# Kernel optimization log

Hardware: AMD Instinct MI355X
Metric: run time of the kernel (lower is better)

The kernel has to match this reference:

```python
import jax, jax.numpy as jnp
import numpy as np

N_NODES = 50000
N_RELS = 100000
N_TRIPLES = 100000
D = 512          # node_dim == rel_dim
H = 768          # hidden_dim
NUM_LAYERS = 3
B = 16           # number of images (segments)
EPS = 1e-5


def setup_inputs() -> dict:
    key = jax.random.key(0)
    ks = jax.random.split(key, 12)
    node_feats = jax.random.normal(ks[0], (N_NODES, D), dtype=jnp.float32)
    rel_feats = jax.random.normal(ks[1], (N_RELS, D), dtype=jnp.float32)
    subj = jax.random.randint(ks[2], (N_TRIPLES,), 0, N_NODES)
    rel = jax.random.randint(ks[3], (N_TRIPLES,), 0, N_RELS)
    obj = jax.random.randint(ks[4], (N_TRIPLES,), 0, N_NODES)
    triples = jnp.stack([subj, rel, obj], axis=1).astype(jnp.int64)
    obj_to_img = jnp.sort(jax.random.randint(ks[5], (N_NODES,), 0, B))
    obj_to_img = obj_to_img.at[-1].set(B - 1)  # pin batch_size = B (torch uses max+1)
    obj_to_img = obj_to_img.astype(jnp.int64)
    s = 0.02
    params = dict(
        node_in_w=jax.random.normal(ks[6], (H, D), dtype=jnp.float32) * s,
        node_in_b=jnp.zeros((H,), dtype=jnp.float32),
        rel_in_w=jax.random.normal(ks[7], (H, D), dtype=jnp.float32) * s,
        rel_in_b=jnp.zeros((H,), dtype=jnp.float32),
        proj_w=jax.random.normal(ks[8], (NUM_LAYERS, H, 2 * H), dtype=jnp.float32) * s,
        proj_b=jnp.zeros((NUM_LAYERS, H), dtype=jnp.float32),
        ln_node_g=jnp.ones((H,), dtype=jnp.float32),
        ln_node_b=jnp.zeros((H,), dtype=jnp.float32),
        ln_rel_g=jnp.ones((H,), dtype=jnp.float32),
        ln_rel_b=jnp.zeros((H,), dtype=jnp.float32),
    )
    return dict(node_feats=node_feats, rel_feats=rel_feats, triples=triples,
                obj_to_img=obj_to_img, **params)


def _layer_norm(x, g, b):
    mu = jnp.mean(x, axis=-1, keepdims=True)
    var = jnp.var(x, axis=-1, keepdims=True)
    return (x - mu) * jax.lax.rsqrt(var + EPS) * g + b


def reference(node_feats, rel_feats, triples, obj_to_img,
              node_in_w, node_in_b, rel_in_w, rel_in_b,
              proj_w, proj_b, ln_node_g, ln_node_b, ln_rel_g, ln_rel_b):
    subj_idx, rel_idx, obj_idx = triples[:, 0], triples[:, 1], triples[:, 2]

    node_states = node_feats @ node_in_w.T + node_in_b          # (N_nodes, H)
    rel_states = rel_feats @ rel_in_w.T + rel_in_b               # (N_rels, H)

    for l in range(NUM_LAYERS):
        rel_g = rel_states[rel_idx]                              # (T, H)
        msg_s2o = node_states[subj_idx] + rel_g                  # subject -> object
        msg_o2s = node_states[obj_idx] + rel_g                   # object -> subject
        agg = (jax.ops.segment_sum(msg_s2o, obj_idx, num_segments=N_NODES)
               + jax.ops.segment_sum(msg_o2s, subj_idx, num_segments=N_NODES))
        h = jnp.concatenate([node_states, agg], axis=-1)         # (N_nodes, 2H)
        h = h @ proj_w[l].T + proj_b[l]
        h = jax.nn.silu(h)
        node_states = node_states + h                            # residual (dropout=0)

    node_states = _layer_norm(node_states, ln_node_g, ln_node_b)
    rel_states = _layer_norm(rel_states, ln_rel_g, ln_rel_b)

    sums = jax.ops.segment_sum(node_states, obj_to_img, num_segments=B)
    counts = jax.ops.segment_sum(jnp.ones((N_NODES,), node_states.dtype),
                                 obj_to_img, num_segments=B)
    global_states = sums / jnp.clip(counts, 1.0)[:, None]        # (B, H)
    return node_states, global_states
```

## Files before the change

### kernel.cpp

```cpp
#include <hip/hip_runtime.h>
#include <hip/hip_bf16.h>
#include <math.h>

#define N_NODES   50000
#define N_RELS    100000
#define N_TRIPLES 100000
#define D_IN      512
#define H_DIM     768
#define NUM_LAYERS 3
#define B_IMG     16
#define MP        50176

typedef __attribute__((ext_vector_type(8))) short short8;
typedef __attribute__((ext_vector_type(4))) float f32x4;

typedef const __attribute__((address_space(1))) unsigned int glb_u32;
typedef __attribute__((address_space(3))) unsigned int lds_u32;

__device__ inline short f2bf16s(float f){
  union { __hip_bfloat16 h; unsigned short u; } cv;
  cv.h = __float2bfloat16(f);
  return (short)cv.u;
}
__device__ inline float bf2f(unsigned short u){
  union { unsigned u; float f; } c; c.u = ((unsigned)u)<<16; return c.f;
}
__device__ inline uint2 pack4bf(float4 v){
  uint2 r;
  r.x = ((unsigned)(unsigned short)f2bf16s(v.x)) | (((unsigned)(unsigned short)f2bf16s(v.y))<<16);
  r.y = ((unsigned)(unsigned short)f2bf16s(v.z)) | (((unsigned)(unsigned short)f2bf16s(v.w))<<16);
  return r;
}
__device__ inline float4 unpack4bf(uint2 p){
  float4 v;
  v.x = bf2f((unsigned short)(p.x & 0xffff)); v.y = bf2f((unsigned short)(p.x >> 16));
  v.z = bf2f((unsigned short)(p.y & 0xffff)); v.w = bf2f((unsigned short)(p.y >> 16));
  return v;
}

__global__ void detect_idx64_kernel(const unsigned* __restrict__ tr, int* __restrict__ flag){
  if (threadIdx.x == 0 && blockIdx.x == 0){
    unsigned o = 0;
    for (int k = 0; k < 256; k++) o |= tr[2*k + 1];
    flag[0] = (o == 0) ? 1 : 0;
  }
}

__device__ inline void load_triple(const void* tp, int t, int is64, int& s, int& r, int& o){
  if (is64){
    const long long* p = (const long long*)tp;
    s = (int)p[3*t]; r = (int)p[3*t+1]; o = (int)p[3*t+2];
  } else {
    const int* p = (const int*)tp;
    s = p[3*t]; r = p[3*t+1]; o = p[3*t+2];
  }
  s = (s < 0) ? 0 : (s >= N_NODES ? N_NODES-1 : s);
  o = (o < 0) ? 0 : (o >= N_NODES ? N_NODES-1 : o);
  r = (r < 0) ? 0 : (r >= N_RELS  ? N_RELS-1  : r);
}

__device__ inline int idx_at(const void* p, int i, int is64){
  return is64 ? (int)((const long long*)p)[i] : ((const int*)p)[i];
}

__global__ __launch_bounds__(256)
void hist_kernel(const void* __restrict__ tr, const int* __restrict__ flag,
                 int* __restrict__ deg){
  int t = blockIdx.x*256 + threadIdx.x;
  if (t >= N_TRIPLES) return;
  int s, r, o;
  load_triple(tr, t, flag[0], s, r, o);
  atomicAdd(&deg[o], 1);
  atomicAdd(&deg[s], 1);
}

__global__ __launch_bounds__(1024)
void scan_kernel(const int* __restrict__ deg, int* __restrict__ offs,
                 int* __restrict__ cursor, float* __restrict__ cnt){
  __shared__ int partial[1024];
  int tid = threadIdx.x;
  const int per = (N_NODES + 1023)/1024;
  int start = tid*per, end = start+per; if (end > N_NODES) end = N_NODES;
  if (start > N_NODES) start = N_NODES;
  int s = 0;
  for (int i=start; i<end; i++) s += deg[i];
  partial[tid] = s;
  __syncthreads();
  for (int off=1; off<1024; off<<=1){
    int v = (tid >= off) ? partial[tid-off] : 0;
    __syncthreads();
    partial[tid] += v;
    __syncthreads();
  }
  int run = (tid > 0) ? partial[tid-1] : 0;
  for (int i=start; i<end; i++){
    offs[i] = run; cursor[i] = run; cnt[i] = (float)deg[i];
    run += deg[i];
  }
  if (tid == 1023) offs[N_NODES] = run;
}

__global__ __launch_bounds__(256)
void fill_kernel(const void* __restrict__ tr, const int* __restrict__ flag,
                 int* __restrict__ cursor, int* __restrict__ col_node,
                 int* __restrict__ col_rel){
  int t = blockIdx.x*256 + threadIdx.x;
  if (t >= N_TRIPLES) return;
  int s, r, o;
  load_triple(tr, t, flag[0], s, r, o);
  int p1 = atomicAdd(&cursor[o], 1); col_node[p1] = s; col_rel[p1] = r;
  int p2 = atomicAdd(&cursor[s], 1); col_node[p2] = o; col_rel[p2] = r;
}

__global__ __launch_bounds__(256)
void gather_rel_kernel(const int* __restrict__ offs, const int* __restrict__ col_rel,
                       const float* __restrict__ relf, unsigned short* __restrict__ rfa_bf){
  int v = blockIdx.x*4 + (threadIdx.x >> 6);
  int lane = threadIdx.x & 63;
  float4 a0 = {0,0,0,0}, a1 = {0,0,0,0};
  int lo = offs[v], hi = offs[v+1];
  for (int e=lo; e<hi; e++){
    int r = col_rel[e];
    const float* rp = relf + (size_t)r*D_IN + lane*4;
    float4 x0 = *(const float4*)rp;
    float4 x1 = *(const float4*)(rp + 256);
    a0.x+=x0.x; a0.y+=x0.y; a0.z+=x0.z; a0.w+=x0.w;
    a1.x+=x1.x; a1.y+=x1.y; a1.z+=x1.z; a1.w+=x1.w;
  }
  uint2* out = (uint2*)(rfa_bf + (size_t)v*D_IN);
  out[lane]    = pack4bf(a0);
  out[lane+64] = pack4bf(a1);
}

__global__ __launch_bounds__(256)
void gather_node_bf_kernel(const int* __restrict__ offs, const int* __restrict__ col_node,
                           const unsigned short* __restrict__ seed_bf,
                           const unsigned short* __restrict__ node_bf,
                           unsigned short* __restrict__ agg_bf){
  int v = blockIdx.x*4 + (threadIdx.x >> 6);
  int lane = threadIdx.x & 63;
  const uint2* sp = (const uint2*)(seed_bf + (size_t)v*H_DIM);
  float4 a0 = unpack4bf(sp[lane]);
  float4 a1 = unpack4bf(sp[lane+64]);
  float4 a2 = unpack4bf(sp[lane+128]);
  int lo = offs[v], hi = offs[v+1];
  for (int e=lo; e<hi; e++){
    int u = col_node[e];
    const uint2* np = (const uint2*)(node_bf + (size_t)u*H_DIM);
    float4 x0 = unpack4bf(np[lane]);
    float4 x1 = unpack4bf(np[lane+64]);
    float4 x2 = unpack4bf(np[lane+128]);
    a0.x+=x0.x; a0.y+=x0.y; a0.z+=x0.z; a0.w+=x0.w;
    a1.x+=x1.x; a1.y+=x1.y; a1.z+=x1.z; a1.w+=x1.w;
    a2.x+=x2.x; a2.y+=x2.y; a2.z+=x2.z; a2.w+=x2.w;
  }
  uint2* out = (uint2*)(agg_bf + (size_t)v*H_DIM);
  out[lane]     = pack4bf(a0);
  out[lane+64]  = pack4bf(a1);
  out[lane+128] = pack4bf(a2);
}

__global__ __launch_bounds__(256)
void gather_node_kernel(const int* __restrict__ offs, const int* __restrict__ col_node,
                        const unsigned short* __restrict__ seed_bf,
                        const float* __restrict__ node,
                        unsigned short* __restrict__ agg_bf){
  int v = blockIdx.x*4 + (threadIdx.x >> 6);
  int lane = threadIdx.x & 63;
  const uint2* sp = (const uint2*)(seed_bf + (size_t)v*H_DIM);
  float4 a0 = unpack4bf(sp[lane]);
  float4 a1 = unpack4bf(sp[lane+64]);
  float4 a2 = unpack4bf(sp[lane+128]);
  int lo = offs[v], hi = offs[v+1];
  for (int e=lo; e<hi; e++){
    int u = col_node[e];
    const float* np = node + (size_t)u*H_DIM + lane*4;
    float4 x0 = *(const float4*)np;
    float4 x1 = *(const float4*)(np + 256);
    float4 x2 = *(const float4*)(np + 512);
    a0.x+=x0.x; a0.y+=x0.y; a0.z+=x0.z; a0.w+=x0.w;
    a1.x+=x1.x; a1.y+=x1.y; a1.z+=x1.z; a1.w+=x1.w;
    a2.x+=x2.x; a2.y+=x2.y; a2.z+=x2.z; a2.w+=x2.w;
  }
  uint2* out = (uint2*)(agg_bf + (size_t)v*H_DIM);
  out[lane]     = pack4bf(a0);
  out[lane+64]  = pack4bf(a1);
  out[lane+128] = pack4bf(a2);
}

__device__ inline short8 load_cvt8(const float* __restrict__ p, bool valid){
  short8 r;
  if (valid){
    float4 v0 = *(const float4*)(p);
    float4 v1 = *(const float4*)(p+4);
    r[0]=f2bf16s(v0.x); r[1]=f2bf16s(v0.y); r[2]=f2bf16s(v0.z); r[3]=f2bf16s(v0.w);
    r[4]=f2bf16s(v1.x); r[5]=f2bf16s(v1.y); r[6]=f2bf16s(v1.z); r[7]=f2bf16s(v1.w);
  } else {
    r = (short8)0;
  }
  return r;
}

template<int MODE>
__global__ __launch_bounds__(512)
void gemm_lds(const unsigned short* __restrict__ A1,
              const unsigned short* __restrict__ A2,
              const unsigned short* __restrict__ W,
              const float* __restrict__ bias,
              const float* __restrict__ rowscale,
              float* __restrict__ Cf,
              unsigned short* __restrict__ Cbf,
              int M, int K1, int K2)
{
  __shared__ unsigned short As[256*64];
  __shared__ unsigned short Bs[128*64];
  const int lane = threadIdx.x & 63;
  const int wv   = threadIdx.x >> 6;
  const int llo  = lane & 15, lhi = lane >> 4;
  const int wm   = (wv>>1)*64;
  const int wn   = (wv&1)*64;

  const int nwg  = gridDim.x;
  const int q8   = nwg >> 3, r8 = nwg & 7;
  const int xcd  = blockIdx.x & 7, base = blockIdx.x >> 3;
  const int virt = (xcd < r8 ? xcd*(q8+1) : r8*(q8+1) + (xcd-r8)*q8) + base;
  const int bm   = (virt / 6) * 256;
  const int bn   = (virt % 6) * 128;
  const int KW   = K1 + K2;

  const int srow = lane >> 3;
  const int scol = ((lane & 7) ^ srow) * 8;

  f32x4 acc[4][4];
  #pragma unroll
  for (int i=0;i<4;i++)
    #pragma unroll
    for (int j=0;j<4;j++) acc[i][j] = (f32x4)(0.0f);

  const unsigned short* Wb = W + (size_t)bn*KW;

  for (int k0=0; k0<KW; k0+=64){
    const unsigned short* Asrc; int ak0, astr;
    if (k0 < K1){ Asrc = A1 + (size_t)bm*K1; ak0 = k0;      astr = K1; }
    else        { Asrc = A2 + (size_t)bm*K2; ak0 = k0 - K1; astr = K2; }
    #pragma unroll
    for (int p=0;p<4;p++){
      int c = wv*4 + p;
      int row = c*8 + srow;
      __builtin_amdgcn_global_load_lds(
        (glb_u32*)(Asrc + (size_t)row*astr + ak0 + scol),
        (lds_u32*)(As + c*512), 16, 0, 0);
    }
    #pragma unroll
    for (int p=0;p<2;p++){
      int c = wv*2 + p;
      int row = c*8 + srow;
      __builtin_amdgcn_global_load_lds(
        (glb_u32*)(Wb + (size_t)row*KW + k0 + scol),
        (lds_u32*)(Bs + c*512), 16, 0, 0);
    }
    __syncthreads();
    #pragma unroll
    for (int kk=0; kk<64; kk+=32){
      short8 a[4], b[4];
      #pragma unroll
      for (int i=0;i<4;i++){
        int rowA = wm + i*16 + llo;
        int rowB = wn + i*16 + llo;
        int c16  = lhi + (kk>>3);
        a[i] = *(const short8*)(As + rowA*64 + ((c16 ^ (rowA&7))*8));
        b[i] = *(const short8*)(Bs + rowB*64 + ((c16 ^ (rowB&7))*8));
      }
      #pragma unroll
      for (int i=0;i<4;i++)
        #pragma unroll
        for (int j=0;j<4;j++)
          acc[i][j] = __builtin_amdgcn_mfma_f32_16x16x32_bf16(a[i], b[j], acc[i][j], 0,0,0);
    }
    __syncthreads();
  }

  #pragma unroll
  for (int j=0;j<4;j++){
    int col = bn + wn + j*16 + llo;
    float bv = bias ? bias[col] : 0.0f;
    #pragma unroll
    for (int i=0;i<4;i++){
      #pragma unroll
      for (int r=0;r<4;r++){
        int row = bm + wm + i*16 + lhi*4 + r;
        if (row < M){
          size_t idx = (size_t)row*H_DIM + col;
          float v = acc[i][j][r];
          if (MODE==0){
            v += bv;
            Cf[idx] = v;
            Cbf[idx] = (unsigned short)f2bf16s(v);
          } else if (MODE==2){
            v += rowscale[row]*bv;
            Cbf[idx] = (unsigned short)f2bf16s(v);
          } else {
            v += bv;
            float s = v / (1.0f + __expf(-v));
            float nv = Cf[idx] + s;
            Cf[idx] = nv;
            Cbf[idx] = (unsigned short)f2bf16s(nv);
          }
        }
      }
    }
  }
}

template<int MODE, int ABF>
__global__ __launch_bounds__(256)
void gemm_in(const float* __restrict__ Xf, const unsigned short* __restrict__ Xbf,
             const unsigned short* __restrict__ W,
             const float* __restrict__ bias, const float* __restrict__ rowscale,
             float* __restrict__ Cf, unsigned short* __restrict__ Cbf,
             int M, int Ka)
{
  const int lane = threadIdx.x & 63;
  const int wv   = threadIdx.x >> 6;
  const int llo  = lane & 15, lhi = lane >> 4;
  const int bm   = blockIdx.x*128 + (wv>>1)*64;
  const int bn   = blockIdx.y*128 + (wv&1)*64;

  f32x4 acc[4][4];
  #pragma unroll
  for (int i=0;i<4;i++)
    #pragma unroll
    for (int j=0;j<4;j++) acc[i][j] = (f32x4)(0.0f);

  for (int k0=0;k0<Ka;k0+=32){
    short8 a[4], b[4];
    #pragma unroll
    for (int i=0;i<4;i++){
      int row = bm + i*16 + llo;
      if (ABF) a[i] = (row < M) ? *(const short8*)(Xbf + (size_t)row*Ka + k0 + lhi*8) : (short8)0;
      else     a[i] = load_cvt8(Xf + (size_t)row*Ka + k0 + lhi*8, row < M);
      b[i] = *(const short8*)(W + (size_t)(bn + i*16 + llo)*Ka + k0 + lhi*8);
    }
    #pragma unroll
    for (int i=0;i<4;i++)
      #pragma unroll
      for (int j=0;j<4;j++)
        acc[i][j] = __builtin_amdgcn_mfma_f32_16x16x32_bf16(a[i], b[j], acc[i][j], 0,0,0);
  }

  #pragma unroll
  for (int j=0;j<4;j++){
    int col = bn + j*16 + llo;
    float bv = bias ? bias[col] : 0.0f;
    #pragma unroll
    for (int i=0;i<4;i++){
      #pragma unroll
      for (int r=0;r<4;r++){
        int row = bm + i*16 + lhi*4 + r;
        if (row < M){
          size_t idx = (size_t)row*H_DIM + col;
          float v = acc[i][j][r];
          if (MODE==2){
            v += rowscale[row]*bv;
            Cbf[idx] = (unsigned short)f2bf16s(v);
          } else {
            Cf[idx] = v + bv;
          }
        }
      }
    }
  }
}

__global__ __launch_bounds__(512)
void gemm_layer(float* __restrict__ node,
                const unsigned short* __restrict__ agg_bf,
                const unsigned short* __restrict__ W,
                const float* __restrict__ bias,
                int M)
{
  const int lane = threadIdx.x & 63;
  const int wv   = threadIdx.x >> 6;
  const int llo  = lane & 15, lhi = lane >> 4;
  const int bm   = blockIdx.x*64;
  const int bn   = wv*96;

  f32x4 acc[4][6];
  #pragma unroll
  for (int i=0;i<4;i++)
    #pragma unroll
    for (int j=0;j<6;j++) acc[i][j] = (f32x4)(0.0f);

  for (int k0=0;k0<H_DIM;k0+=32){
    short8 a[4], b[6];
    #pragma unroll
    for (int i=0;i<4;i++){
      int row = bm + i*16 + llo;
      a[i] = load_cvt8(node + (size_t)row*H_DIM + k0 + lhi*8, row < M);
    }
    #pragma unroll
    for (int j=0;j<6;j++)
      b[j] = *(const short8*)(W + (size_t)(bn + j*16 + llo)*(2*H_DIM) + k0 + lhi*8);
    #pragma unroll
    for (int i=0;i<4;i++)
      #pragma unroll
      for (int j=0;j<6;j++)
        acc[i][j] = __builtin_amdgcn_mfma_f32_16x16x32_bf16(a[i], b[j], acc[i][j], 0,0,0);
  }
  for (int k0=0;k0<H_DIM;k0+=32){
    short8 a[4], b[6];
    #pragma unroll
    for (int i=0;i<4;i++){
      int row = bm + i*16 + llo;
      a[i] = (row < M) ? *(const short8*)(agg_bf + (size_t)row*H_DIM + k0 + lhi*8) : (short8)0;
    }
    #pragma unroll
    for (int j=0;j<6;j++)
      b[j] = *(const short8*)(W + (size_t)(bn + j*16 + llo)*(2*H_DIM) + H_DIM + k0 + lhi*8);
    #pragma unroll
    for (int i=0;i<4;i++)
      #pragma unroll
      for (int j=0;j<6;j++)
        acc[i][j] = __builtin_amdgcn_mfma_f32_16x16x32_bf16(a[i], b[j], acc[i][j], 0,0,0);
  }

  __syncthreads();

  #pragma unroll
  for (int j=0;j<6;j++){
    int col = bn + j*16 + llo;
    float bv = bias[col];
    #pragma unroll
    for (int i=0;i<4;i++){
      #pragma unroll
      for (int r=0;r<4;r++){
        int row = bm + i*16 + lhi*4 + r;
        if (row < M){
          size_t idx = (size_t)row*H_DIM + col;
          float v = acc[i][j][r] + bv;
          float s = v / (1.0f + __expf(-v));
          node[idx] += s;
        }
      }
    }
  }
}

__global__ __launch_bounds__(256)
void cast_bf16_kernel(const float* __restrict__ src, unsigned short* __restrict__ dst,
                      long n){
  long i = ((long)blockIdx.x*blockDim.x + threadIdx.x)*8;
  long stride = (long)gridDim.x*blockDim.x*8;
  for (; i < n; i += stride){
    float4 v0 = *(const float4*)(src+i);
    float4 v1 = *(const float4*)(src+i+4);
    short8 o;
    o[0]=f2bf16s(v0.x); o[1]=f2bf16s(v0.y); o[2]=f2bf16s(v0.z); o[3]=f2bf16s(v0.w);
    o[4]=f2bf16s(v1.x); o[5]=f2bf16s(v1.y); o[6]=f2bf16s(v1.z); o[7]=f2bf16s(v1.w);
    *(short8*)(dst+i) = o;
  }
}

__global__ __launch_bounds__(256)
void ln_kernel(const float* __restrict__ x, const float* __restrict__ g,
               const float* __restrict__ b, float* __restrict__ out){
  int row = blockIdx.x;
  int t = threadIdx.x;
  const float* xr = x + (size_t)row*H_DIM;
  float v0 = xr[t], v1 = xr[t+256], v2 = xr[t+512];
  float s  = v0+v1+v2;
  float ss = v0*v0+v1*v1+v2*v2;
  for (int off=32; off>0; off>>=1){
    s  += __shfl_down(s,  off);
    ss += __shfl_down(ss, off);
  }
  __shared__ float rs_[4], rss_[4];
  __shared__ float mu_s, rstd_s;
  int lane = t & 63, wv = t >> 6;
  if (lane==0){ rs_[wv]=s; rss_[wv]=ss; }
  __syncthreads();
  if (t==0){
    float S  = rs_[0]+rs_[1]+rs_[2]+rs_[3];
    float SS = rss_[0]+rss_[1]+rss_[2]+rss_[3];
    float mu = S * (1.0f/768.0f);
    float var = SS * (1.0f/768.0f) - mu*mu;
    mu_s = mu; rstd_s = rsqrtf(var + 1e-5f);
  }
  __syncthreads();
  float mu = mu_s, rstd = rstd_s;
  float* orow = out + (size_t)row*H_DIM;
  orow[t]     = (v0-mu)*rstd*g[t]     + b[t];
  orow[t+256] = (v1-mu)*rstd*g[t+256] + b[t+256];
  orow[t+512] = (v2-mu)*rstd*g[t+512] + b[t+512];
}

__global__ __launch_bounds__(256)
void pool1_kernel(const float* __restrict__ ln, const void* __restrict__ o2i,
                  const int* __restrict__ flag, float* __restrict__ acc){
  const int ROWS = 125;
  int is64 = flag[0];
  int r0 = blockIdx.x*ROWS;
  int t = threadIdx.x;
  float a0=0.f, a1=0.f, a2=0.f;
  int cur = idx_at(o2i, r0, is64);
  cur = (cur < 0) ? 0 : (cur >= B_IMG ? B_IMG-1 : cur);
  for (int r=r0; r<r0+ROWS; r++){
    int img = idx_at(o2i, r, is64);
    img = (img < 0) ? 0 : (img >= B_IMG ? B_IMG-1 : img);
    if (img != cur){
      atomicAdd(&acc[cur*H_DIM + t],       a0);
      atomicAdd(&acc[cur*H_DIM + t + 256], a1);
      atomicAdd(&acc[cur*H_DIM + t + 512], a2);
      a0 = a1 = a2 = 0.f;
      cur = img;
    }
    const float* xr = ln + (size_t)r*H_DIM;
    a0 += xr[t]; a1 += xr[t+256]; a2 += xr[t+512];
  }
  atomicAdd(&acc[cur*H_DIM + t],       a0);
  atomicAdd(&acc[cur*H_DIM + t + 256], a1);
  atomicAdd(&acc[cur*H_DIM + t + 512], a2);
}

__device__ inline int lbound_idx(const void* a, int n, int v, int is64){
  int lo=0, hi=n;
  while (lo<hi){ int m=(lo+hi)>>1; if (idx_at(a,m,is64) < v) lo=m+1; else hi=m; }
  return lo;
}

__global__ __launch_bounds__(256)
void pool2_kernel(const float* __restrict__ acc, const void* __restrict__ o2i,
                  const int* __restrict__ flag, float* __restrict__ gout){
  int is64 = flag[0];
  int img = blockIdx.x;
  int t = threadIdx.x;
  int lo = lbound_idx(o2i, N_NODES, img,   is64);
  int hi = lbound_idx(o2i, N_NODES, img+1, is64);
  float c = (float)(hi-lo);
  if (c < 1.0f) c = 1.0f;
  float inv = 1.0f / c;
  gout[(size_t)img*H_DIM + t]       = acc[img*H_DIM + t]       * inv;
  gout[(size_t)img*H_DIM + t + 256] = acc[img*H_DIM + t + 256] * inv;
  gout[(size_t)img*H_DIM + t + 512] = acc[img*H_DIM + t + 512] * inv;
}

extern "C" void kernel_launch(void* const* d_in, const int* in_sizes, int n_in,
                              void* d_out, int out_size, void* d_ws, size_t ws_size,
                              hipStream_t stream){
  const float* node_feats = (const float*)d_in[0];
  const float* rel_feats  = (const float*)d_in[1];
  const void*  triples    = d_in[2];
  const void*  o2i        = d_in[3];
  const float* node_in_w  = (const float*)d_in[4];
  const float* node_in_b  = (const float*)d_in[5];
  const float* rel_in_w   = (const float*)d_in[6];
  const float* rel_in_b   = (const float*)d_in[7];
  const float* proj_w     = (const float*)d_in[8];
  const float* proj_b     = (const float*)d_in[9];
  const float* ln_g       = (const float*)d_in[10];
  const float* ln_b       = (const float*)d_in[11];

  float* out_nodes  = (float*)d_out;
  float* out_global = (float*)d_out + (size_t)N_NODES*H_DIM;

  const int  tri_blocks = (N_TRIPLES + 255)/256;
  const int  gat_blocks = N_NODES/4;

  size_t off = 0;
  auto alloc = [&](size_t bytes)->void*{
    void* r = (char*)d_ws + off; off += (bytes + 255) & ~(size_t)255; return r;
  };
  unsigned short* w_node     = (unsigned short*)alloc((size_t)H_DIM*D_IN*2);
  unsigned short* w_rel      = (unsigned short*)alloc((size_t)H_DIM*D_IN*2);
  unsigned short* w_proj     = (unsigned short*)alloc((size_t)NUM_LAYERS*H_DIM*2*H_DIM*2);
  unsigned short* rel_agg_bf = (unsigned short*)alloc((size_t)MP*H_DIM*2);
  unsigned short* shr_bf     = (unsigned short*)alloc((size_t)MP*D_IN*2);
  unsigned short* node_bf0   = (unsigned short*)alloc((size_t)MP*H_DIM*2);
  unsigned short* node_bf1   = (unsigned short*)alloc((size_t)MP*H_DIM*2);
  unsigned short* agg_bf     = (unsigned short*)alloc((size_t)MP*H_DIM*2);
  float*          cnt        = (float*)alloc((size_t)N_NODES*4);
  int*            deg        = (int*)alloc((size_t)N_NODES*4);
  int*            offs       = (int*)alloc((size_t)(N_NODES+1)*4);
  int*            cursor     = (int*)alloc((size_t)N_NODES*4);
  int*            col_node   = (int*)alloc((size_t)2*N_TRIPLES*4);
  int*            col_rel    = (int*)alloc((size_t)2*N_TRIPLES*4);
  int*            flag       = (int*)alloc(256);
  float*          pool_acc   = (float*)alloc((size_t)B_IMG*H_DIM*4);
  size_t need_full = off;

  detect_idx64_kernel<<<1,64,0,stream>>>((const unsigned*)triples, flag);
  hipMemsetAsync(deg, 0, (size_t)N_NODES*4, stream);
  hist_kernel<<<tri_blocks,256,0,stream>>>(triples, flag, deg);
  scan_kernel<<<1,1024,0,stream>>>(deg, offs, cursor, cnt);
  fill_kernel<<<tri_blocks,256,0,stream>>>(triples, flag, cursor, col_node, col_rel);
  cast_bf16_kernel<<<512,256,0,stream>>>(node_in_w, w_node, (long)H_DIM*D_IN);
  cast_bf16_kernel<<<512,256,0,stream>>>(rel_in_w,  w_rel,  (long)H_DIM*D_IN);
  cast_bf16_kernel<<<2048,256,0,stream>>>(proj_w, w_proj, (long)NUM_LAYERS*H_DIM*2*H_DIM);

  if (ws_size >= need_full){
    const int gg = (MP/256) * (H_DIM/128);

    cast_bf16_kernel<<<2048,256,0,stream>>>(node_feats, shr_bf, (long)N_NODES*D_IN);
    gemm_lds<0><<<gg,512,0,stream>>>(shr_bf, nullptr, w_node, node_in_b, nullptr,
                                     out_nodes, node_bf0, N_NODES, D_IN, 0);

    gather_rel_kernel<<<gat_blocks,256,0,stream>>>(offs, col_rel, rel_feats, shr_bf);
    gemm_lds<2><<<gg,512,0,stream>>>(shr_bf, nullptr, w_rel, rel_in_b, cnt,
                                     nullptr, rel_agg_bf, N_NODES, D_IN, 0);

    unsigned short* cur = node_bf0;
    unsigned short* nxt = node_bf1;
    for (int l=0; l<NUM_LAYERS; ++l){
      gather_node_bf_kernel<<<gat_blocks,256,0,stream>>>(offs, col_node, rel_agg_bf,
                                                         cur, agg_bf);
      gemm_lds<1><<<gg,512,0,stream>>>(cur, agg_bf,
                                       w_proj + (size_t)l*H_DIM*2*H_DIM,
                                       proj_b + (size_t)l*H_DIM, nullptr,
                                       out_nodes, nxt, N_NODES, H_DIM, H_DIM);
      unsigned short* t = cur; cur = nxt; nxt = t;
    }
  } else {
    size_t off2 = 0;
    auto alloc2 = [&](size_t bytes)->void*{
      void* r = (char*)d_ws + off2; off2 += (bytes + 255) & ~(size_t)255; return r;
    };
    unsigned short* w_node2  = (unsigned short*)alloc2((size_t)H_DIM*D_IN*2);
    unsigned short* w_rel2   = (unsigned short*)alloc2((size_t)H_DIM*D_IN*2);
    unsigned short* w_proj2  = (unsigned short*)alloc2((size_t)NUM_LAYERS*H_DIM*2*H_DIM*2);
    unsigned short* relagg2  = (unsigned short*)alloc2((size_t)N_NODES*H_DIM*2);
    unsigned short* rfa2     = (unsigned short*)alloc2((size_t)N_NODES*D_IN*2);
    unsigned short* agg2     = (unsigned short*)alloc2((size_t)N_NODES*H_DIM*2);
    float* cnt2   = (float*)alloc2((size_t)N_NODES*4);
    int*   deg2   = (int*)alloc2((size_t)N_NODES*4);
    int*   offs2  = (int*)alloc2((size_t)(N_NODES+1)*4);
    int*   cur2   = (int*)alloc2((size_t)N_NODES*4);
    int*   coln2  = (int*)alloc2((size_t)2*N_TRIPLES*4);
    int*   colr2  = (int*)alloc2((size_t)2*N_TRIPLES*4);
    int*   flag2  = (int*)alloc2(256);
    float* pacc2  = (float*)alloc2((size_t)B_IMG*H_DIM*4);
    if (ws_size < off2) return;

    detect_idx64_kernel<<<1,64,0,stream>>>((const unsigned*)triples, flag2);
    hipMemsetAsync(deg2, 0, (size_t)N_NODES*4, stream);
    hist_kernel<<<tri_blocks,256,0,stream>>>(triples, flag2, deg2);
    scan_kernel<<<1,1024,0,stream>>>(deg2, offs2, cur2, cnt2);
    fill_kernel<<<tri_blocks,256,0,stream>>>(triples, flag2, cur2, coln2, colr2);
    cast_bf16_kernel<<<512,256,0,stream>>>(node_in_w, w_node2, (long)H_DIM*D_IN);
    cast_bf16_kernel<<<512,256,0,stream>>>(rel_in_w,  w_rel2,  (long)H_DIM*D_IN);
    cast_bf16_kernel<<<2048,256,0,stream>>>(proj_w, w_proj2, (long)NUM_LAYERS*H_DIM*2*H_DIM);

    const dim3 gemm_grid((N_NODES + 127)/128, H_DIM/128);
    gemm_in<0,0><<<gemm_grid,256,0,stream>>>(node_feats, nullptr, w_node2, node_in_b, nullptr,
                                             out_nodes, nullptr, N_NODES, D_IN);
    gather_rel_kernel<<<gat_blocks,256,0,stream>>>(offs2, colr2, rel_feats, rfa2);
    gemm_in<2,1><<<gemm_grid,256,0,stream>>>(nullptr, rfa2, w_rel2, rel_in_b, cnt2,
                                             nullptr, relagg2, N_NODES, D_IN);
    for (int l=0; l<NUM_LAYERS; ++l){
      gather_node_kernel<<<gat_blocks,256,0,stream>>>(offs2, coln2, relagg2,
                                                      out_nodes, agg2);
      gemm_layer<<<(N_NODES+63)/64,512,0,stream>>>(out_nodes, agg2,
                                                   w_proj2 + (size_t)l*H_DIM*2*H_DIM,
                                                   proj_b + (size_t)l*H_DIM, N_NODES);
    }
    flag = flag2; pool_acc = pacc2;
  }

  ln_kernel<<<N_NODES,256,0,stream>>>(out_nodes, ln_g, ln_b, out_nodes);
  hipMemsetAsync(pool_acc, 0, (size_t)B_IMG*H_DIM*4, stream);
  pool1_kernel<<<400,256,0,stream>>>(out_nodes, o2i, flag, pool_acc);
  pool2_kernel<<<B_IMG,256,0,stream>>>(pool_acc, o2i, flag, out_global);
}
```

Measured before the change: 1.687 ms.

## Keep node states in bf16 only and pre-cast relation features for gather

Drops the fp32 node-state buffer in the main path. GEMM epilogues now write only bf16, and the residual is read back from the bf16 input. The final layernorm reads the bf16 states. Relation features are cast to bf16 once before the gather, which halves the bytes read by the irregular gather, at the cost of an extra full cast pass over 100k×512 floats. Carrying the residual stream only in bf16 across layers adds rounding error that accumulates.

```diff
diff --git a/kernel.cpp b/kernel.cpp
--- a/kernel.cpp
+++ b/kernel.cpp
@@ -110,6 +110,27 @@
   load_triple(tr, t, flag[0], s, r, o);
   int p1 = atomicAdd(&cursor[o], 1); col_node[p1] = s; col_rel[p1] = r;
   int p2 = atomicAdd(&cursor[s], 1); col_node[p2] = o; col_rel[p2] = r;
+}
+
+__global__ __launch_bounds__(256)
+void gather_rel_bf_kernel(const int* __restrict__ offs, const int* __restrict__ col_rel,
+                          const unsigned short* __restrict__ relf_bf,
+                          unsigned short* __restrict__ rfa_bf){
+  int v = blockIdx.x*4 + (threadIdx.x >> 6);
+  int lane = threadIdx.x & 63;
+  float4 a0 = {0,0,0,0}, a1 = {0,0,0,0};
+  int lo = offs[v], hi = offs[v+1];
+  for (int e=lo; e<hi; e++){
+    int r = col_rel[e];
+    const uint2* rp = (const uint2*)(relf_bf + (size_t)r*D_IN);
+    float4 x0 = unpack4bf(rp[lane]);
+    float4 x1 = unpack4bf(rp[lane+64]);
+    a0.x+=x0.x; a0.y+=x0.y; a0.z+=x0.z; a0.w+=x0.w;
+    a1.x+=x1.x; a1.y+=x1.y; a1.z+=x1.z; a1.w+=x1.w;
+  }
+  uint2* out = (uint2*)(rfa_bf + (size_t)v*D_IN);
+  out[lane]    = pack4bf(a0);
+  out[lane+64] = pack4bf(a1);
 }
 
 __global__ __launch_bounds__(256)
@@ -208,7 +229,6 @@
               const unsigned short* __restrict__ W,
               const float* __restrict__ bias,
               const float* __restrict__ rowscale,
-              float* __restrict__ Cf,
               unsigned short* __restrict__ Cbf,
               int M, int K1, int K2)
 {
@@ -293,17 +313,14 @@
           size_t idx = (size_t)row*H_DIM + col;
           float v = acc[i][j][r];
           if (MODE==0){
-            v += bv;
-            Cf[idx] = v;
-            Cbf[idx] = (unsigned short)f2bf16s(v);
+            Cbf[idx] = (unsigned short)f2bf16s(v + bv);
           } else if (MODE==2){
             v += rowscale[row]*bv;
             Cbf[idx] = (unsigned short)f2bf16s(v);
           } else {
             v += bv;
             float s = v / (1.0f + __expf(-v));
-            float nv = Cf[idx] + s;
-            Cf[idx] = nv;
+            float nv = bf2f(A1[idx]) + s;
             Cbf[idx] = (unsigned short)f2bf16s(nv);
           }
         }
@@ -468,6 +485,39 @@
   int t = threadIdx.x;
   const float* xr = x + (size_t)row*H_DIM;
   float v0 = xr[t], v1 = xr[t+256], v2 = xr[t+512];
+  float s  = v0+v1+v2;
+  float ss = v0*v0+v1*v1+v2*v2;
+  for (int off=32; off>0; off>>=1){
+    s  += __shfl_down(s,  off);
+    ss += __shfl_down(ss, off);
+  }
+  __shared__ float rs_[4], rss_[4];
+  __shared__ float mu_s, rstd_s;
+  int lane = t & 63, wv = t >> 6;
+  if (lane==0){ rs_[wv]=s; rss_[wv]=ss; }
+  __syncthreads();
+  if (t==0){
+    float S  = rs_[0]+rs_[1]+rs_[2]+rs_[3];
+    float SS = rss_[0]+rss_[1]+rss_[2]+rss_[3];
+    float mu = S * (1.0f/768.0f);
+    float var = SS * (1.0f/768.0f) - mu*mu;
+    mu_s = mu; rstd_s = rsqrtf(var + 1e-5f);
+  }
+  __syncthreads();
+  float mu = mu_s, rstd = rstd_s;
+  float* orow = out + (size_t)row*H_DIM;
+  orow[t]     = (v0-mu)*rstd*g[t]     + b[t];
+  orow[t+256] = (v1-mu)*rstd*g[t+256] + b[t+256];
+  orow[t+512] = (v2-mu)*rstd*g[t+512] + b[t+512];
+}
+
+__global__ __launch_bounds__(256)
+void ln_bf_kernel(const unsigned short* __restrict__ xbf, const float* __restrict__ g,
+                  const float* __restrict__ b, float* __restrict__ out){
+  int row = blockIdx.x;
+  int t = threadIdx.x;
+  const unsigned short* xr = xbf + (size_t)row*H_DIM;
+  float v0 = bf2f(xr[t]), v1 = bf2f(xr[t+256]), v2 = bf2f(xr[t+512]);
   float s  = v0+v1+v2;
   float ss = v0*v0+v1*v1+v2*v2;
   for (int off=32; off>0; off>>=1){
@@ -574,6 +624,7 @@
   unsigned short* w_rel      = (unsigned short*)alloc((size_t)H_DIM*D_IN*2);
   unsigned short* w_proj     = (unsigned short*)alloc((size_t)NUM_LAYERS*H_DIM*2*H_DIM*2);
   unsigned short* rel_agg_bf = (unsigned short*)alloc((size_t)MP*H_DIM*2);
+  unsigned short* relf_bf    = (unsigned short*)alloc((size_t)N_RELS*D_IN*2);
   unsigned short* shr_bf     = (unsigned short*)alloc((size_t)MP*D_IN*2);
   unsigned short* node_bf0   = (unsigned short*)alloc((size_t)MP*H_DIM*2);
   unsigned short* node_bf1   = (unsigned short*)alloc((size_t)MP*H_DIM*2);
@@ -602,11 +653,12 @@
 
     cast_bf16_kernel<<<2048,256,0,stream>>>(node_feats, shr_bf, (long)N_NODES*D_IN);
     gemm_lds<0><<<gg,512,0,stream>>>(shr_bf, nullptr, w_node, node_in_b, nullptr,
-                                     out_nodes, node_bf0, N_NODES, D_IN, 0);
-
-    gather_rel_kernel<<<gat_blocks,256,0,stream>>>(offs, col_rel, rel_feats, shr_bf);
+                                     node_bf0, N_NODES, D_IN, 0);
+
+    cast_bf16_kernel<<<2048,256,0,stream>>>(rel_feats, relf_bf, (long)N_RELS*D_IN);
+    gather_rel_bf_kernel<<<gat_blocks,256,0,stream>>>(offs, col_rel, relf_bf, shr_bf);
     gemm_lds<2><<<gg,512,0,stream>>>(shr_bf, nullptr, w_rel, rel_in_b, cnt,
-                                     nullptr, rel_agg_bf, N_NODES, D_IN, 0);
+                                     rel_agg_bf, N_NODES, D_IN, 0);
 
     unsigned short* cur = node_bf0;
     unsigned short* nxt = node_bf1;
@@ -616,9 +668,14 @@
       gemm_lds<1><<<gg,512,0,stream>>>(cur, agg_bf,
                                        w_proj + (size_t)l*H_DIM*2*H_DIM,
                                        proj_b + (size_t)l*H_DIM, nullptr,
-                                       out_nodes, nxt, N_NODES, H_DIM, H_DIM);
+                                       nxt, N_NODES, H_DIM, H_DIM);
       unsigned short* t = cur; cur = nxt; nxt = t;
     }
+
+    ln_bf_kernel<<<N_NODES,256,0,stream>>>(cur, ln_g, ln_b, out_nodes);
+    hipMemsetAsync(pool_acc, 0, (size_t)B_IMG*H_DIM*4, stream);
+    pool1_kernel<<<400,256,0,stream>>>(out_nodes, o2i, flag, pool_acc);
+    pool2_kernel<<<B_IMG,256,0,stream>>>(pool_acc, o2i, flag, out_global);
   } else {
     size_t off2 = 0;
     auto alloc2 = [&](size_t bytes)->void*{
@@ -662,11 +719,10 @@
                                                    w_proj2 + (size_t)l*H_DIM*2*H_DIM,
                                                    proj_b + (size_t)l*H_DIM, N_NODES);
     }
-    flag = flag2; pool_acc = pacc2;
-  }
-
-  ln_kernel<<<N_NODES,256,0,stream>>>(out_nodes, ln_g, ln_b, out_nodes);
-  hipMemsetAsync(pool_acc, 0, (size_t)B_IMG*H_DIM*4, stream);
-  pool1_kernel<<<400,256,0,stream>>>(out_nodes, o2i, flag, pool_acc);
-  pool2_kernel<<<B_IMG,256,0,stream>>>(pool_acc, o2i, flag, out_global);
-}
+
+    ln_kernel<<<N_NODES,256,0,stream>>>(out_nodes, ln_g, ln_b, out_nodes);
+    hipMemsetAsync(pacc2, 0, (size_t)B_IMG*H_DIM*4, stream);
+    pool1_kernel<<<400,256,0,stream>>>(out_nodes, o2i, flag2, pacc2);
+    pool2_kernel<<<B_IMG,256,0,stream>>>(pacc2, o2i, flag2, out_global);
+  }
+}
```

After: 1.455 ms (median of 3 runs). 1.16x faster.
